# Optimization experiments

Measured on AMD Instinct MI355X. Metric: run time of the kernel, lower is better.

The kernel has to match this reference:

```python
import jax, jax.numpy as jnp
import numpy as np

N_NODES = 100000
N_EDGES = 1600000
IN_DIM = 768
HIDDEN = 256
N_CLASSES = 3


def setup_inputs() -> dict:
    key = jax.random.key(0)
    k0, k1, k2, k3 = jax.random.split(key, 4)
    x = jax.random.normal(k0, (N_NODES, IN_DIM), dtype=jnp.float32)
    edge_index = jax.random.randint(k1, (2, N_EDGES), 0, N_NODES, dtype=jnp.int32)
    # Glorot-ish init for weights
    W1 = jax.random.normal(k2, (IN_DIM, HIDDEN), dtype=jnp.float32) * (1.0 / np.sqrt(IN_DIM))
    b1 = jnp.zeros((HIDDEN,), dtype=jnp.float32)
    W2 = jax.random.normal(k3, (HIDDEN, N_CLASSES), dtype=jnp.float32) * (1.0 / np.sqrt(HIDDEN))
    b2 = jnp.zeros((N_CLASSES,), dtype=jnp.float32)
    return {"x": x, "edge_index": edge_index, "W1": W1, "b1": b1, "W2": W2, "b2": b2}


def reference(x, edge_index, W1, b1, W2, b2):
    """dumb_GNN forward: GCNConv(768->H) -> relu -> (dropout=eval identity) -> Linear -> log_softmax.

    GCNConv math (PyG default): out = D^{-1/2} (A + I) D^{-1/2} X W + b
    """
    n = x.shape[0]
    src, dst = edge_index[0], edge_index[1]
    # add self-loops
    loops = jnp.arange(n, dtype=src.dtype)
    src = jnp.concatenate([src, loops])
    dst = jnp.concatenate([dst, loops])
    # symmetric degree normalization (degrees include self-loops)
    deg = jax.ops.segment_sum(jnp.ones_like(src, dtype=x.dtype), dst, num_segments=n)
    dinv = jnp.where(deg > 0, jax.lax.rsqrt(deg), jnp.zeros_like(deg))
    norm = dinv[src] * dinv[dst]  # [E+N]
    # transform then gather-scale-scatter aggregate
    h = x @ W1  # [N, H]
    agg = jax.ops.segment_sum(h[src] * norm[:, None], dst, num_segments=n) + b1
    h = jax.nn.relu(agg)
    # dropout is identity at inference
    logits = h @ W2 + b2  # [N, C]
    return jax.nn.log_softmax(logits, axis=-1)
```

## Files before the change

### kernel.cpp

```cpp
#include <hip/hip_runtime.h>
#include <hip/hip_bf16.h>
#include <math.h>

#define N_NODES 100000
#define N_EDGES 1600000
#define IN_DIM  768
#define HIDDEN  256

#define SCAN_B  256
#define N_SBLK  ((N_NODES + SCAN_B - 1) / SCAN_B)

#define H_OFF    0ull
#define ADJ_OFF  51200000ull
#define RS_OFF   57600000ull
#define CUR_OFF  58000016ull
#define DEG_OFF  58400016ull
#define DINV_OFF 58800016ull
#define W1T_OFF  59200016ull
#define BSUM_OFF 59593232ull

typedef short          bf16x8 __attribute__((ext_vector_type(8)));
typedef float          fp32x4 __attribute__((ext_vector_type(4)));
typedef unsigned short u16x4  __attribute__((ext_vector_type(4)));

__device__ inline short f2bf(float f) {
    union { float f; unsigned u; } c; c.f = f;
    unsigned u = c.u;
    unsigned r = u + 0x7FFFu + ((u >> 16) & 1u);
    return (short)(r >> 16);
}

__device__ inline fp32x4 bf4_to_f4(u16x4 v) {
    fp32x4 r;
    for (int j = 0; j < 4; j++) {
        union { unsigned u; float f; } c;
        c.u = ((unsigned)v[j]) << 16;
        r[j] = c.f;
    }
    return r;
}

__global__ void init_kernel(int* __restrict__ deg, int* __restrict__ cursor) {
    int i = blockIdx.x * blockDim.x + threadIdx.x;
    if (i < N_NODES) { deg[i] = 0; cursor[i] = 0; }
}

__global__ void w1t_kernel(const float* __restrict__ w1, short* __restrict__ w1t) {
    int i = blockIdx.x * blockDim.x + threadIdx.x;
    if (i < HIDDEN * IN_DIM) {
        int n = i / IN_DIM, k = i % IN_DIM;
        w1t[i] = f2bf(w1[(size_t)k * HIDDEN + n]);
    }
}

__global__ void count_kernel(const int* __restrict__ dst, int* __restrict__ deg) {
    int e = blockIdx.x * blockDim.x + threadIdx.x;
    if (e < N_EDGES) atomicAdd(&deg[dst[e]], 1);
}

__global__ __launch_bounds__(SCAN_B) void scan1_kernel(const int* __restrict__ deg,
                                                       int* __restrict__ bsum) {
    int i = blockIdx.x * SCAN_B + threadIdx.x;
    int v = (i < N_NODES) ? deg[i] : 0;
    for (int off = 32; off > 0; off >>= 1) v += __shfl_down(v, off, 64);
    __shared__ int wsum[SCAN_B / 64];
    int lane = threadIdx.x & 63, w = threadIdx.x >> 6;
    if (lane == 0) wsum[w] = v;
    __syncthreads();
    if (threadIdx.x == 0) {
        int s = 0;
        for (int j = 0; j < SCAN_B / 64; j++) s += wsum[j];
        bsum[blockIdx.x] = s;
    }
}

__global__ __launch_bounds__(512) void scan2_kernel(int* __restrict__ bsum) {
    __shared__ int s[512];
    int tid = threadIdx.x;
    int v = (tid < N_SBLK) ? bsum[tid] : 0;
    s[tid] = v;
    __syncthreads();
    for (int off = 1; off < 512; off <<= 1) {
        int t = (tid >= off) ? s[tid - off] : 0;
        __syncthreads();
        s[tid] += t;
        __syncthreads();
    }
    if (tid < N_SBLK) bsum[tid] = s[tid] - v;
}

__global__ __launch_bounds__(SCAN_B) void scan3_kernel(const int* __restrict__ deg,
                                                       const int* __restrict__ bsum,
                                                       int* __restrict__ row_start,
                                                       float* __restrict__ dinv) {
    __shared__ int s[SCAN_B];
    int i = blockIdx.x * SCAN_B + threadIdx.x;
    int tid = threadIdx.x;
    int d = (i < N_NODES) ? deg[i] : 0;
    s[tid] = d;
    __syncthreads();
    for (int off = 1; off < SCAN_B; off <<= 1) {
        int t = (tid >= off) ? s[tid - off] : 0;
        __syncthreads();
        s[tid] += t;
        __syncthreads();
    }
    if (i < N_NODES) {
        row_start[i] = bsum[blockIdx.x] + s[tid] - d;
        dinv[i] = rsqrtf((float)(d + 1));
        if (i == N_NODES - 1) row_start[N_NODES] = N_EDGES;
    }
}

__global__ void fill_kernel(const int* __restrict__ src, const int* __restrict__ dst,
                            const int* __restrict__ row_start, int* __restrict__ cursor,
                            int* __restrict__ adj) {
    int e = blockIdx.x * blockDim.x + threadIdx.x;
    if (e < N_EDGES) {
        int d = dst[e];
        int p = row_start[d] + atomicAdd(&cursor[d], 1);
        adj[p] = src[e];
    }
}

__global__ __launch_bounds__(256) void gemm1_kernel(const float* __restrict__ x,
                                                    const short* __restrict__ w1t,
                                                    const float* __restrict__ dinv,
                                                    unsigned short* __restrict__ h) {
    __shared__ short a_lds[128][40];
    __shared__ short b_lds[128][40];

    const int tid  = threadIdx.x;
    const int lane = tid & 63;
    const int wave = tid >> 6;
    const int wm = (wave >> 1) * 64;
    const int wn = (wave & 1) * 64;
    const int l15 = lane & 15;
    const int q   = lane >> 4;
    const int row0 = blockIdx.x * 128;
    const int col0 = blockIdx.y * 128;

    const int sr0 = tid >> 2;
    const int sr1 = 64 + (tid >> 2);
    const int skk = (tid & 3) * 8;
    const int gr0 = row0 + sr0;
    const int gr1 = row0 + sr1;
    const float* xp0 = x + (size_t)gr0 * IN_DIM + skk;
    const float* xp1 = x + (size_t)gr1 * IN_DIM + skk;
    const short* wp0 = w1t + (size_t)(col0 + sr0) * IN_DIM + skk;
    const short* wp1 = w1t + (size_t)(col0 + sr1) * IN_DIM + skk;
    const bool ok0 = gr0 < N_NODES;
    const bool ok1 = gr1 < N_NODES;

    fp32x4 acc[4][4];
    for (int i = 0; i < 4; i++)
        for (int j = 0; j < 4; j++)
            for (int r = 0; r < 4; r++) acc[i][j][r] = 0.0f;

    fp32x4 pa0a = {0,0,0,0}, pa0b = {0,0,0,0}, pa1a = {0,0,0,0}, pa1b = {0,0,0,0};
    bf16x8 pb0, pb1;

    if (ok0) { pa0a = *(const fp32x4*)xp0; pa0b = *(const fp32x4*)(xp0 + 4); }
    if (ok1) { pa1a = *(const fp32x4*)xp1; pa1b = *(const fp32x4*)(xp1 + 4); }
    pb0 = *(const bf16x8*)wp0;
    pb1 = *(const bf16x8*)wp1;

    for (int k0 = 0; k0 < IN_DIM; k0 += 32) {
        bf16x8 av;
        av[0] = f2bf(pa0a[0]); av[1] = f2bf(pa0a[1]);
        av[2] = f2bf(pa0a[2]); av[3] = f2bf(pa0a[3]);
        av[4] = f2bf(pa0b[0]); av[5] = f2bf(pa0b[1]);
        av[6] = f2bf(pa0b[2]); av[7] = f2bf(pa0b[3]);
        *(bf16x8*)(&a_lds[sr0][skk]) = av;
        av[0] = f2bf(pa1a[0]); av[1] = f2bf(pa1a[1]);
        av[2] = f2bf(pa1a[2]); av[3] = f2bf(pa1a[3]);
        av[4] = f2bf(pa1b[0]); av[5] = f2bf(pa1b[1]);
        av[6] = f2bf(pa1b[2]); av[7] = f2bf(pa1b[3]);
        *(bf16x8*)(&a_lds[sr1][skk]) = av;
        *(bf16x8*)(&b_lds[sr0][skk]) = pb0;
        *(bf16x8*)(&b_lds[sr1][skk]) = pb1;
        __syncthreads();

        int kn = k0 + 32;
        if (kn < IN_DIM) {
            if (ok0) { pa0a = *(const fp32x4*)(xp0 + kn); pa0b = *(const fp32x4*)(xp0 + kn + 4); }
            if (ok1) { pa1a = *(const fp32x4*)(xp1 + kn); pa1b = *(const fp32x4*)(xp1 + kn + 4); }
            pb0 = *(const bf16x8*)(wp0 + kn);
            pb1 = *(const bf16x8*)(wp1 + kn);
        }

        bf16x8 af[4], bfr[4];
        for (int mt = 0; mt < 4; mt++)
            af[mt] = *(const bf16x8*)(&a_lds[wm + mt * 16 + l15][q * 8]);
        for (int nt = 0; nt < 4; nt++)
            bfr[nt] = *(const bf16x8*)(&b_lds[wn + nt * 16 + l15][q * 8]);
        for (int mt = 0; mt < 4; mt++)
            for (int nt = 0; nt < 4; nt++)
                acc[mt][nt] = __builtin_amdgcn_mfma_f32_16x16x32_bf16(
                    af[mt], bfr[nt], acc[mt][nt], 0, 0, 0);
        __syncthreads();
    }

    float dv[4][4];
    for (int mt = 0; mt < 4; mt++)
        for (int r = 0; r < 4; r++) {
            int row = row0 + wm + mt * 16 + q * 4 + r;
            dv[mt][r] = (row < N_NODES) ? dinv[row] : 0.0f;
        }
    for (int mt = 0; mt < 4; mt++) {
        for (int nt = 0; nt < 4; nt++) {
            int col = col0 + wn + nt * 16 + l15;
            for (int r = 0; r < 4; r++) {
                int row = row0 + wm + mt * 16 + q * 4 + r;
                if (row < N_NODES)
                    h[(size_t)row * HIDDEN + col] =
                        (unsigned short)f2bf(dv[mt][r] * acc[mt][nt][r]);
            }
        }
    }
}

__global__ __launch_bounds__(256) void aggregate_kernel(
    const unsigned short* __restrict__ h, const int* __restrict__ adj,
    const int* __restrict__ row_start, const float* __restrict__ dinv,
    const float* __restrict__ b1, const float* __restrict__ w2,
    const float* __restrict__ b2, float* __restrict__ out) {
    const int lane = threadIdx.x & 63;
    const int wave = threadIdx.x >> 6;
    const int v = blockIdx.x * 4 + wave;
    if (v >= N_NODES) return;

    const size_t loff = (size_t)lane * 4;

    fp32x4 a0 = bf4_to_f4(*(const u16x4*)(h + (size_t)v * HIDDEN + loff));
    fp32x4 a1 = {0,0,0,0}, a2 = {0,0,0,0}, a3 = {0,0,0,0};

    int e0 = row_start[v], e1 = row_start[v + 1];
    for (int e = e0; e < e1; e += 64) {
        int cnt = min(64, e1 - e);
        int s = (lane < cnt) ? adj[e + lane] : 0;
        int i = 0;
        for (; i + 4 <= cnt; i += 4) {
            int s0 = __shfl(s, i,     64);
            int s1 = __shfl(s, i + 1, 64);
            int s2 = __shfl(s, i + 2, 64);
            int s3 = __shfl(s, i + 3, 64);
            u16x4 r0 = *(const u16x4*)(h + (size_t)s0 * HIDDEN + loff);
            u16x4 r1 = *(const u16x4*)(h + (size_t)s1 * HIDDEN + loff);
            u16x4 r2 = *(const u16x4*)(h + (size_t)s2 * HIDDEN + loff);
            u16x4 r3 = *(const u16x4*)(h + (size_t)s3 * HIDDEN + loff);
            a0 += bf4_to_f4(r0);
            a1 += bf4_to_f4(r1);
            a2 += bf4_to_f4(r2);
            a3 += bf4_to_f4(r3);
        }
        for (; i < cnt; i++) {
            int si = __shfl(s, i, 64);
            a0 += bf4_to_f4(*(const u16x4*)(h + (size_t)si * HIDDEN + loff));
        }
    }
    fp32x4 acc = (a0 + a1) + (a2 + a3);

    float dvv = dinv[v];
    fp32x4 bb = *(const fp32x4*)(b1 + loff);
    float hr[4];
    for (int j = 0; j < 4; j++) hr[j] = fmaxf(0.0f, dvv * acc[j] + bb[j]);

    float p0 = 0.f, p1 = 0.f, p2 = 0.f;
    for (int j = 0; j < 4; j++) {
        const float* wr = w2 + (size_t)(lane * 4 + j) * 3;
        p0 += hr[j] * wr[0];
        p1 += hr[j] * wr[1];
        p2 += hr[j] * wr[2];
    }
    for (int off = 32; off > 0; off >>= 1) {
        p0 += __shfl_down(p0, off, 64);
        p1 += __shfl_down(p1, off, 64);
        p2 += __shfl_down(p2, off, 64);
    }
    if (lane == 0) {
        p0 += b2[0]; p1 += b2[1]; p2 += b2[2];
        float m = fmaxf(p0, fmaxf(p1, p2));
        float l = logf(expf(p0 - m) + expf(p1 - m) + expf(p2 - m));
        out[(size_t)v * 3 + 0] = p0 - m - l;
        out[(size_t)v * 3 + 1] = p1 - m - l;
        out[(size_t)v * 3 + 2] = p2 - m - l;
    }
}

extern "C" void kernel_launch(void* const* d_in, const int* in_sizes, int n_in,
                              void* d_out, int out_size, void* d_ws, size_t ws_size,
                              hipStream_t stream) {
    const float* x    = (const float*)d_in[0];
    const int*   ei   = (const int*)d_in[1];
    const float* W1   = (const float*)d_in[2];
    const float* b1   = (const float*)d_in[3];
    const float* W2   = (const float*)d_in[4];
    const float* b2   = (const float*)d_in[5];
    float* out = (float*)d_out;

    const int* src = ei;
    const int* dst = ei + N_EDGES;

    char* ws = (char*)d_ws;
    unsigned short* h_ws = (unsigned short*)(ws + H_OFF);
    int*   adj       = (int*)(ws + ADJ_OFF);
    int*   row_start = (int*)(ws + RS_OFF);
    int*   cursor    = (int*)(ws + CUR_OFF);
    int*   deg       = (int*)(ws + DEG_OFF);
    float* dinv      = (float*)(ws + DINV_OFF);
    short* w1t       = (short*)(ws + W1T_OFF);
    int*   bsum      = (int*)(ws + BSUM_OFF);

    init_kernel<<<(N_NODES + 255) / 256, 256, 0, stream>>>(deg, cursor);
    w1t_kernel<<<(HIDDEN * IN_DIM + 255) / 256, 256, 0, stream>>>(W1, w1t);
    count_kernel<<<(N_EDGES + 255) / 256, 256, 0, stream>>>(dst, deg);
    scan1_kernel<<<N_SBLK, SCAN_B, 0, stream>>>(deg, bsum);
    scan2_kernel<<<1, 512, 0, stream>>>(bsum);
    scan3_kernel<<<N_SBLK, SCAN_B, 0, stream>>>(deg, bsum, row_start, dinv);
    fill_kernel<<<(N_EDGES + 255) / 256, 256, 0, stream>>>(src, dst, row_start, cursor, adj);
    gemm1_kernel<<<dim3((N_NODES + 127) / 128, HIDDEN / 128), 256, 0, stream>>>(x, w1t, dinv, h_ws);
    aggregate_kernel<<<N_NODES / 4, 256, 0, stream>>>(h_ws, adj, row_start, dinv, b1, W2, b2, out);
}
```

Before: 779.1 us.

## Stream GEMM1 tiles into double-buffered LDS via direct global-to-LDS loads

The register-staged prefetch in gemm1 is replaced by direct global-to-LDS asynchronous loads (global_load_lds) into double-buffered shared tiles, and an XOR swizzle is applied to avoid bank conflicts. X is now kept as fp32 in LDS and converted to bf16 only when fragments are read, so each tile is converted once per wave that reads it. This aims to overlap the next tile's load with the MFMA work and to cut VGPR pressure and the per-iteration barrier count. The cost is twice the LDS footprint for A plus repeated conversion work, and correctness depends on the async loads having landed by the single barrier per iteration.

```diff
diff --git a/kernel.cpp b/kernel.cpp
--- a/kernel.cpp
+++ b/kernel.cpp
@@ -38,6 +38,13 @@
         r[j] = c.f;
     }
     return r;
+}
+
+__device__ inline void async16(const void* g, void* l) {
+    __builtin_amdgcn_global_load_lds(
+        (const __attribute__((address_space(1))) unsigned int*)g,
+        (__attribute__((address_space(3))) unsigned int*)l,
+        16, 0, 0);
 }
 
 __global__ void init_kernel(int* __restrict__ deg, int* __restrict__ cursor) {
@@ -127,8 +134,8 @@
                                                     const short* __restrict__ w1t,
                                                     const float* __restrict__ dinv,
                                                     unsigned short* __restrict__ h) {
-    __shared__ short a_lds[128][40];
-    __shared__ short b_lds[128][40];
+    __shared__ float a_lds[2][128 * 32];
+    __shared__ short b_lds[2][128 * 32];
 
     const int tid  = threadIdx.x;
     const int lane = tid & 63;
@@ -140,76 +147,103 @@
     const int row0 = blockIdx.x * 128;
     const int col0 = blockIdx.y * 128;
 
-    const int sr0 = tid >> 2;
-    const int sr1 = 64 + (tid >> 2);
-    const int skk = (tid & 3) * 8;
-    const int gr0 = row0 + sr0;
-    const int gr1 = row0 + sr1;
-    const float* xp0 = x + (size_t)gr0 * IN_DIM + skk;
-    const float* xp1 = x + (size_t)gr1 * IN_DIM + skk;
-    const short* wp0 = w1t + (size_t)(col0 + sr0) * IN_DIM + skk;
-    const short* wp1 = w1t + (size_t)(col0 + sr1) * IN_DIM + skk;
-    const bool ok0 = gr0 < N_NODES;
-    const bool ok1 = gr1 < N_NODES;
+    const float* ag[4];
+    int alo[4];
+#pragma unroll
+    for (int i = 0; i < 4; i++) {
+        int cd = (wave * 4 + i) * 64 + lane;
+        int ar = cd >> 3;
+        int asrc = (cd & 7) ^ (ar & 7);
+        int grow = row0 + ar;
+        if (grow >= N_NODES) grow = N_NODES - 1;
+        ag[i]  = x + (size_t)grow * IN_DIM + asrc * 4;
+        alo[i] = cd * 16;
+    }
+    const short* bg[2];
+    int blo[2];
+#pragma unroll
+    for (int i = 0; i < 2; i++) {
+        int cd = (wave * 2 + i) * 64 + lane;
+        int br = cd >> 2;
+        int bsrc = (cd & 3) ^ ((br >> 1) & 3);
+        bg[i]  = w1t + (size_t)(col0 + br) * IN_DIM + bsrc * 8;
+        blo[i] = cd * 16;
+    }
 
     fp32x4 acc[4][4];
+#pragma unroll
     for (int i = 0; i < 4; i++)
+#pragma unroll
         for (int j = 0; j < 4; j++)
+#pragma unroll
             for (int r = 0; r < 4; r++) acc[i][j][r] = 0.0f;
 
-    fp32x4 pa0a = {0,0,0,0}, pa0b = {0,0,0,0}, pa1a = {0,0,0,0}, pa1b = {0,0,0,0};
-    bf16x8 pb0, pb1;
-
-    if (ok0) { pa0a = *(const fp32x4*)xp0; pa0b = *(const fp32x4*)(xp0 + 4); }
-    if (ok1) { pa1a = *(const fp32x4*)xp1; pa1b = *(const fp32x4*)(xp1 + 4); }
-    pb0 = *(const bf16x8*)wp0;
-    pb1 = *(const bf16x8*)wp1;
-
+#define STAGE(buf, k0) do {                                                   \
+        char* ab = (char*)a_lds[buf];                                         \
+        char* bb = (char*)b_lds[buf];                                         \
+        async16(ag[0] + (k0), ab + alo[0]);                                   \
+        async16(ag[1] + (k0), ab + alo[1]);                                   \
+        async16(ag[2] + (k0), ab + alo[2]);                                   \
+        async16(ag[3] + (k0), ab + alo[3]);                                   \
+        async16(bg[0] + (k0), bb + blo[0]);                                   \
+        async16(bg[1] + (k0), bb + blo[1]);                                   \
+    } while (0)
+
+    STAGE(0, 0);
+    __syncthreads();
+
+    int cur = 0;
     for (int k0 = 0; k0 < IN_DIM; k0 += 32) {
-        bf16x8 av;
-        av[0] = f2bf(pa0a[0]); av[1] = f2bf(pa0a[1]);
-        av[2] = f2bf(pa0a[2]); av[3] = f2bf(pa0a[3]);
-        av[4] = f2bf(pa0b[0]); av[5] = f2bf(pa0b[1]);
-        av[6] = f2bf(pa0b[2]); av[7] = f2bf(pa0b[3]);
-        *(bf16x8*)(&a_lds[sr0][skk]) = av;
-        av[0] = f2bf(pa1a[0]); av[1] = f2bf(pa1a[1]);
-        av[2] = f2bf(pa1a[2]); av[3] = f2bf(pa1a[3]);
-        av[4] = f2bf(pa1b[0]); av[5] = f2bf(pa1b[1]);
-        av[6] = f2bf(pa1b[2]); av[7] = f2bf(pa1b[3]);
-        *(bf16x8*)(&a_lds[sr1][skk]) = av;
-        *(bf16x8*)(&b_lds[sr0][skk]) = pb0;
-        *(bf16x8*)(&b_lds[sr1][skk]) = pb1;
-        __syncthreads();
-
         int kn = k0 + 32;
-        if (kn < IN_DIM) {
-            if (ok0) { pa0a = *(const fp32x4*)(xp0 + kn); pa0b = *(const fp32x4*)(xp0 + kn + 4); }
-            if (ok1) { pa1a = *(const fp32x4*)(xp1 + kn); pa1b = *(const fp32x4*)(xp1 + kn + 4); }
-            pb0 = *(const bf16x8*)(wp0 + kn);
-            pb1 = *(const bf16x8*)(wp1 + kn);
-        }
+        if (kn < IN_DIM) STAGE(cur ^ 1, kn);
 
         bf16x8 af[4], bfr[4];
+#pragma unroll
+        for (int mt = 0; mt < 4; mt++) {
+            int ar = wm + mt * 16 + l15;
+            const float* ap = &a_lds[cur][ar * 32];
+            int c0 = (2 * q) ^ (ar & 7);
+            fp32x4 f0 = *(const fp32x4*)(ap + (c0 << 2));
+            fp32x4 f1 = *(const fp32x4*)(ap + ((c0 ^ 1) << 2));
+            bf16x8 av;
+            av[0] = f2bf(f0[0]); av[1] = f2bf(f0[1]);
+            av[2] = f2bf(f0[2]); av[3] = f2bf(f0[3]);
+            av[4] = f2bf(f1[0]); av[5] = f2bf(f1[1]);
+            av[6] = f2bf(f1[2]); av[7] = f2bf(f1[3]);
+            af[mt] = av;
+        }
+#pragma unroll
+        for (int nt = 0; nt < 4; nt++) {
+            int br = wn + nt * 16 + l15;
+            int bs = q ^ ((br >> 1) & 3);
+            bfr[nt] = *(const bf16x8*)(&b_lds[cur][br * 32 + bs * 8]);
+        }
+#pragma unroll
         for (int mt = 0; mt < 4; mt++)
-            af[mt] = *(const bf16x8*)(&a_lds[wm + mt * 16 + l15][q * 8]);
-        for (int nt = 0; nt < 4; nt++)
-            bfr[nt] = *(const bf16x8*)(&b_lds[wn + nt * 16 + l15][q * 8]);
-        for (int mt = 0; mt < 4; mt++)
+#pragma unroll
             for (int nt = 0; nt < 4; nt++)
                 acc[mt][nt] = __builtin_amdgcn_mfma_f32_16x16x32_bf16(
                     af[mt], bfr[nt], acc[mt][nt], 0, 0, 0);
-        __syncthreads();
-    }
+
+        __syncthreads();
+        cur ^= 1;
+    }
+#undef STAGE
 
     float dv[4][4];
+#pragma unroll
     for (int mt = 0; mt < 4; mt++)
+#pragma unroll
         for (int r = 0; r < 4; r++) {
             int row = row0 + wm + mt * 16 + q * 4 + r;
             dv[mt][r] = (row < N_NODES) ? dinv[row] : 0.0f;
         }
+#pragma unroll
     for (int mt = 0; mt < 4; mt++) {
+#pragma unroll
         for (int nt = 0; nt < 4; nt++) {
             int col = col0 + wn + nt * 16 + l15;
+#pragma unroll
             for (int r = 0; r < 4; r++) {
                 int row = row0 + wm + mt * 16 + q * 4 + r;
                 if (row < N_NODES)
```

Result: no change. 783.6 us (+0.6%).
